# Performance work log

Measured on AMD Instinct MI355X. Metric: run time of the kernel, lower is better.

Reference implementation:

```python
import jax, jax.numpy as jnp
import numpy as np

NEG_BIG = -1e10
EPS = 1e-12  # F.normalize default eps


def l2_normalize(x, axis=-1):
    # matches torch.nn.functional.normalize(x): x / max(||x||_2, eps)
    n = jnp.sqrt(jnp.sum(x * x, axis=axis, keepdims=True))
    return x / jnp.maximum(n, EPS)


def setup_inputs() -> dict:
    key = jax.random.key(0)
    k1, k2, k3 = jax.random.split(key, 3)
    B, S, T, D, R = 16, 512, 512, 512, 8
    return {
        "src_emb": jax.random.normal(k1, (B, S, D), dtype=jnp.float32),
        "tar_emb": jax.random.normal(k2, (B, T, D), dtype=jnp.float32),
        "src_mask": jnp.ones((B, S), dtype=jnp.float32),
        "tar_mask": jnp.ones((B, T), dtype=jnp.float32),
        "mul_score_w": jax.random.normal(k3, (R, D), dtype=jnp.float32),
    }


def reference(src_emb, tar_emb, src_mask, tar_mask, mul_score_w):
    # w: [R, D] row-normalized relation vectors
    w = l2_normalize(mul_score_w, axis=-1)
    # rank-1 diagonal projections per relation
    src_wt = jnp.einsum("bsd,rd->brs", src_emb, w)          # [B,R,S]
    tar_wt = jnp.einsum("btd,rd->brt", tar_emb, w)          # [B,R,T]
    src_map = src_wt[..., None] * w[None, :, None, :]        # [B,R,S,D]
    tar_map = tar_wt[..., None] * w[None, :, None, :]        # [B,R,T,D]
    # attention scores per relation
    score = jnp.einsum("brsd,brtd->brst", src_map, tar_map)  # [B,R,S,T]
    pair_mask = src_mask[:, :, None] * tar_mask[:, None, :]  # [B,S,T]
    score = score + ((1.0 - pair_mask) * NEG_BIG)[:, None, :, :]
    weight = jax.nn.softmax(score, axis=3)                   # softmax over tar
    # sum over rel and tar in one contraction (avoids 5D tensor)
    out = jnp.einsum("brst,brtd->bsd", weight, tar_map)      # [B,S,D]
    return out
```

## Files before the change

kernel.cpp:

```cpp
#include <hip/hip_runtime.h>
#include <hip/hip_bf16.h>
#include <math.h>

#define B 16
#define Sn 512
#define Tn 512
#define Dn 512
#define Rn 8
#define NEG_BIG (-1e10f)

__device__ __forceinline__ float wred_sum(float v) {
#pragma unroll
  for (int off = 32; off; off >>= 1) v += __shfl_xor(v, off, 64);
  return v;
}
__device__ __forceinline__ float wred_max(float v) {
#pragma unroll
  for (int off = 32; off; off >>= 1) v = fmaxf(v, __shfl_xor(v, off, 64));
  return v;
}

__device__ __forceinline__ void stage_norm_w(const float* __restrict__ w,
                                             float4* w4n, float* gs) {
  const float4* wg = (const float4*)w;
  int wid = threadIdx.x >> 6, lane = threadIdx.x & 63;
  int base = wid * 256;
  float4 g0 = wg[base + lane];
  float4 g1 = wg[base + 64 + lane];
  float4 g2 = wg[base + 128 + lane];
  float4 g3 = wg[base + 192 + lane];
  float ss0 = g0.x * g0.x + g0.y * g0.y + g0.z * g0.z + g0.w * g0.w +
              g1.x * g1.x + g1.y * g1.y + g1.z * g1.z + g1.w * g1.w;
  float ss1 = g2.x * g2.x + g2.y * g2.y + g2.z * g2.z + g2.w * g2.w +
              g3.x * g3.x + g3.y * g3.y + g3.z * g3.z + g3.w * g3.w;
  ss0 = wred_sum(ss0);
  ss1 = wred_sum(ss1);
  float inv0 = 1.0f / fmaxf(sqrtf(ss0), 1e-12f);
  float inv1 = 1.0f / fmaxf(sqrtf(ss1), 1e-12f);
  float4 o;
  o.x = g0.x * inv0; o.y = g0.y * inv0; o.z = g0.z * inv0; o.w = g0.w * inv0;
  w4n[base + lane] = o;
  o.x = g1.x * inv0; o.y = g1.y * inv0; o.z = g1.z * inv0; o.w = g1.w * inv0;
  w4n[base + 64 + lane] = o;
  o.x = g2.x * inv1; o.y = g2.y * inv1; o.z = g2.z * inv1; o.w = g2.w * inv1;
  w4n[base + 128 + lane] = o;
  o.x = g3.x * inv1; o.y = g3.y * inv1; o.z = g3.z * inv1; o.w = g3.w * inv1;
  w4n[base + 192 + lane] = o;
  if (lane == 0) {
    gs[2 * wid] = ss0 * inv0 * inv0;
    gs[2 * wid + 1] = ss1 * inv1 * inv1;
  }
}

__global__ __launch_bounds__(256) void proj_kernel(
    const float* __restrict__ src_emb, const float* __restrict__ tar_emb,
    const float* __restrict__ w, float* __restrict__ src_wt,
    float* __restrict__ tar_wt) {
  __shared__ float4 w4n[Rn * 128];
  __shared__ float gs[Rn];
  stage_norm_w(w, w4n, gs);
  __syncthreads();

  bool is_src = blockIdx.x < 2048;
  const float* emb = is_src ? src_emb : tar_emb;
  float* wt = is_src ? src_wt : tar_wt;
  int bb = is_src ? blockIdx.x : blockIdx.x - 2048;

  int wid = threadIdx.x >> 6, lane = threadIdx.x & 63;
  int row = bb * 4 + wid;
  const float4* e4 = (const float4*)(emb + (size_t)row * Dn);
  float4 xa = e4[lane];
  float4 xb = e4[lane + 64];

  float p[8];
#pragma unroll
  for (int r = 0; r < 8; ++r) {
    float4 wa = w4n[r * 128 + lane];
    float4 wb = w4n[r * 128 + 64 + lane];
    p[r] = xa.x * wa.x + xa.y * wa.y + xa.z * wa.z + xa.w * wa.w +
           xb.x * wb.x + xb.y * wb.y + xb.z * wb.z + xb.w * wb.w;
  }
#pragma unroll
  for (int off = 32; off; off >>= 1) {
#pragma unroll
    for (int r = 0; r < 8; ++r) p[r] += __shfl_xor(p[r], off, 64);
  }
  if (lane == 0) {
    int b = row >> 9, n = row & 511;
#pragma unroll
    for (int r = 0; r < 8; ++r) wt[(((size_t)b * Rn + r) << 9) + n] = p[r];
  }
}

__global__ __launch_bounds__(256) void fused_kernel(
    const float* __restrict__ src_wt, const float* __restrict__ tar_wt,
    const float* __restrict__ src_mask, const float* __restrict__ tar_mask,
    const float* __restrict__ w, float* __restrict__ out) {
  __shared__ float4 w4n[Rn * 128];
  __shared__ float gs[Rn];
  __shared__ float sw_s[Rn][8];
  __shared__ float sm_s[8];

  int b = blockIdx.x >> 6;
  int s0 = (blockIdx.x & 63) * 8;

  stage_norm_w(w, w4n, gs);
  if (threadIdx.x < 64) {
    int r = threadIdx.x >> 3, si = threadIdx.x & 7;
    sw_s[r][si] = src_wt[(((size_t)b * Rn + r) << 9) + s0 + si];
    if (r == 0) sm_s[si] = src_mask[((size_t)b << 9) + s0 + si];
  }
  __syncthreads();

  int wid = threadIdx.x >> 6, lane = threadIdx.x & 63;

  const float4* twb = (const float4*)(tar_wt + ((size_t)b << 12));
  float4 tw[8][2];
#pragma unroll
  for (int r = 0; r < 8; ++r) {
    tw[r][0] = twb[r * 128 + lane];
    tw[r][1] = twb[r * 128 + 64 + lane];
  }
  const float4* tmb = (const float4*)(tar_mask + ((size_t)b << 9));
  float4 tm0 = tmb[lane], tm1 = tmb[lane + 64];
  float gr[8];
#pragma unroll
  for (int r = 0; r < 8; ++r) gr[r] = gs[r];

#pragma unroll
  for (int it = 0; it < 2; ++it) {
    int sl = wid * 2 + it;
    int s = s0 + sl;
    float sm = sm_s[sl];
    float mk[8];
    mk[0] = (1.0f - sm * tm0.x) * NEG_BIG;
    mk[1] = (1.0f - sm * tm0.y) * NEG_BIG;
    mk[2] = (1.0f - sm * tm0.z) * NEG_BIG;
    mk[3] = (1.0f - sm * tm0.w) * NEG_BIG;
    mk[4] = (1.0f - sm * tm1.x) * NEG_BIG;
    mk[5] = (1.0f - sm * tm1.y) * NEG_BIG;
    mk[6] = (1.0f - sm * tm1.z) * NEG_BIG;
    mk[7] = (1.0f - sm * tm1.w) * NEG_BIG;

    float cacc[8];
#pragma unroll
    for (int r = 0; r < 8; ++r) {
      float a = gr[r] * sw_s[r][sl];
      float twv[8] = {tw[r][0].x, tw[r][0].y, tw[r][0].z, tw[r][0].w,
                      tw[r][1].x, tw[r][1].y, tw[r][1].z, tw[r][1].w};
      float sc[8];
      float m = -INFINITY;
#pragma unroll
      for (int k = 0; k < 8; ++k) {
        sc[k] = a * twv[k] + mk[k];
        m = fmaxf(m, sc[k]);
      }
      m = wred_max(m);
      float ps = 0.f, wsum = 0.f;
#pragma unroll
      for (int k = 0; k < 8; ++k) {
        float p = __expf(sc[k] - m);
        ps += p;
        wsum += p * twv[k];
      }
      ps = wred_sum(ps);
      wsum = wred_sum(wsum);
      cacc[r] = wsum / ps;
    }

    float4 o0 = {0, 0, 0, 0}, o1 = {0, 0, 0, 0};
#pragma unroll
    for (int r = 0; r < 8; ++r) {
      float4 wa = w4n[r * 128 + lane];
      float4 wb = w4n[r * 128 + 64 + lane];
      o0.x += cacc[r] * wa.x; o0.y += cacc[r] * wa.y;
      o0.z += cacc[r] * wa.z; o0.w += cacc[r] * wa.w;
      o1.x += cacc[r] * wb.x; o1.y += cacc[r] * wb.y;
      o1.z += cacc[r] * wb.z; o1.w += cacc[r] * wb.w;
    }
    float4* dst = (float4*)(out + (((size_t)b << 9) + s) * Dn);
    dst[lane] = o0;
    dst[lane + 64] = o1;
  }
}

extern "C" void kernel_launch(void* const* d_in, const int* in_sizes, int n_in,
                              void* d_out, int out_size, void* d_ws,
                              size_t ws_size, hipStream_t stream) {
  const float* src_emb = (const float*)d_in[0];
  const float* tar_emb = (const float*)d_in[1];
  const float* src_mask = (const float*)d_in[2];
  const float* tar_mask = (const float*)d_in[3];
  const float* w_in = (const float*)d_in[4];
  float* out = (float*)d_out;

  float* ws = (float*)d_ws;
  float* src_wt = ws;
  float* tar_wt = ws + 65536;

  proj_kernel<<<4096, 256, 0, stream>>>(src_emb, tar_emb, w_in, src_wt, tar_wt);
  fused_kernel<<<B * 64, 256, 0, stream>>>(src_wt, tar_wt, src_mask, tar_mask,
                                           w_in, out);
}
```

Baseline: 116.8 us.

## Rewrite projection and softmax kernels with bound-based max and register weights

Both kernels are restructured. The projection kernel handles four rows per wave, keeps the normalized weights in registers instead of LDS, uses a folding shuffle reduction across the 8 relations, and writes a [row, R] layout. The fused kernel stages target projections in LDS, replaces the per-row max reduction with an analytic upper bound |a|*max|tw| so softmax needs one pass with exp2, and gives each lane one (s, r) pair looping over T. This removes many cross-lane max/sum reductions and LDS traffic. The bound-based shift could underflow when |a|*M is large, and each block now recomputes the weight normalization redundantly.

```diff
diff --git a/kernel.cpp b/kernel.cpp
--- a/kernel.cpp
+++ b/kernel.cpp
@@ -8,47 +8,61 @@
 #define Dn 512
 #define Rn 8
 #define NEG_BIG (-1e10f)
-
-__device__ __forceinline__ float wred_sum(float v) {
-#pragma unroll
-  for (int off = 32; off; off >>= 1) v += __shfl_xor(v, off, 64);
+#define L2E 1.4426950408889634f
+
+__device__ __forceinline__ float dot4(float4 a, float4 b) {
+  return a.x * b.x + a.y * b.y + a.z * b.z + a.w * b.w;
+}
+
+__device__ __forceinline__ float fold_reduce8(const float* p, int lane) {
+  bool b0 = lane & 1;
+  float q[4];
+#pragma unroll
+  for (int j = 0; j < 4; ++j) {
+    float s = b0 ? p[2 * j] : p[2 * j + 1];
+    float rv = __shfl_xor(s, 1, 64);
+    q[j] = (b0 ? p[2 * j + 1] : p[2 * j]) + rv;
+  }
+  bool b1 = lane & 2;
+  float u[2];
+#pragma unroll
+  for (int j = 0; j < 2; ++j) {
+    float s = b1 ? q[2 * j] : q[2 * j + 1];
+    float rv = __shfl_xor(s, 2, 64);
+    u[j] = (b1 ? q[2 * j + 1] : q[2 * j]) + rv;
+  }
+  bool b2 = lane & 4;
+  float s = b2 ? u[0] : u[1];
+  float rv = __shfl_xor(s, 4, 64);
+  float v = (b2 ? u[1] : u[0]) + rv;
+  v += __shfl_xor(v, 8, 64);
+  v += __shfl_xor(v, 16, 64);
+  v += __shfl_xor(v, 32, 64);
   return v;
 }
-__device__ __forceinline__ float wred_max(float v) {
-#pragma unroll
-  for (int off = 32; off; off >>= 1) v = fmaxf(v, __shfl_xor(v, off, 64));
-  return v;
-}
-
-__device__ __forceinline__ void stage_norm_w(const float* __restrict__ w,
-                                             float4* w4n, float* gs) {
+
+__device__ __forceinline__ void load_norm_w(const float* __restrict__ w,
+                                            int lane, float4* wa, float4* wb,
+                                            float* g) {
   const float4* wg = (const float4*)w;
-  int wid = threadIdx.x >> 6, lane = threadIdx.x & 63;
-  int base = wid * 256;
-  float4 g0 = wg[base + lane];
-  float4 g1 = wg[base + 64 + lane];
-  float4 g2 = wg[base + 128 + lane];
-  float4 g3 = wg[base + 192 + lane];
-  float ss0 = g0.x * g0.x + g0.y * g0.y + g0.z * g0.z + g0.w * g0.w +
-              g1.x * g1.x + g1.y * g1.y + g1.z * g1.z + g1.w * g1.w;
-  float ss1 = g2.x * g2.x + g2.y * g2.y + g2.z * g2.z + g2.w * g2.w +
-              g3.x * g3.x + g3.y * g3.y + g3.z * g3.z + g3.w * g3.w;
-  ss0 = wred_sum(ss0);
-  ss1 = wred_sum(ss1);
-  float inv0 = 1.0f / fmaxf(sqrtf(ss0), 1e-12f);
-  float inv1 = 1.0f / fmaxf(sqrtf(ss1), 1e-12f);
-  float4 o;
-  o.x = g0.x * inv0; o.y = g0.y * inv0; o.z = g0.z * inv0; o.w = g0.w * inv0;
-  w4n[base + lane] = o;
-  o.x = g1.x * inv0; o.y = g1.y * inv0; o.z = g1.z * inv0; o.w = g1.w * inv0;
-  w4n[base + 64 + lane] = o;
-  o.x = g2.x * inv1; o.y = g2.y * inv1; o.z = g2.z * inv1; o.w = g2.w * inv1;
-  w4n[base + 128 + lane] = o;
-  o.x = g3.x * inv1; o.y = g3.y * inv1; o.z = g3.z * inv1; o.w = g3.w * inv1;
-  w4n[base + 192 + lane] = o;
-  if (lane == 0) {
-    gs[2 * wid] = ss0 * inv0 * inv0;
-    gs[2 * wid + 1] = ss1 * inv1 * inv1;
+  float ss[8];
+#pragma unroll
+  for (int r = 0; r < 8; ++r) {
+    wa[r] = wg[r * 128 + lane];
+    wb[r] = wg[r * 128 + 64 + lane];
+    ss[r] = dot4(wa[r], wa[r]) + dot4(wb[r], wb[r]);
+  }
+#pragma unroll
+  for (int off = 32; off; off >>= 1) {
+#pragma unroll
+    for (int r = 0; r < 8; ++r) ss[r] += __shfl_xor(ss[r], off, 64);
+  }
+#pragma unroll
+  for (int r = 0; r < 8; ++r) {
+    float iv = 1.0f / fmaxf(sqrtf(ss[r]), 1e-12f);
+    wa[r].x *= iv; wa[r].y *= iv; wa[r].z *= iv; wa[r].w *= iv;
+    wb[r].x *= iv; wb[r].y *= iv; wb[r].z *= iv; wb[r].w *= iv;
+    g[r] = ss[r] * iv * iv;
   }
 }
 
@@ -56,39 +70,32 @@
     const float* __restrict__ src_emb, const float* __restrict__ tar_emb,
     const float* __restrict__ w, float* __restrict__ src_wt,
     float* __restrict__ tar_wt) {
-  __shared__ float4 w4n[Rn * 128];
-  __shared__ float gs[Rn];
-  stage_norm_w(w, w4n, gs);
-  __syncthreads();
-
-  bool is_src = blockIdx.x < 2048;
+  int lane = threadIdx.x & 63, wid = threadIdx.x >> 6;
+  float4 wa[8], wb[8];
+  float g[8];
+  load_norm_w(w, lane, wa, wb, g);
+
+  int row0 = blockIdx.x * 16 + wid * 4;
+  bool is_src = row0 < B * Sn;
   const float* emb = is_src ? src_emb : tar_emb;
   float* wt = is_src ? src_wt : tar_wt;
-  int bb = is_src ? blockIdx.x : blockIdx.x - 2048;
-
-  int wid = threadIdx.x >> 6, lane = threadIdx.x & 63;
-  int row = bb * 4 + wid;
-  const float4* e4 = (const float4*)(emb + (size_t)row * Dn);
-  float4 xa = e4[lane];
-  float4 xb = e4[lane + 64];
-
-  float p[8];
-#pragma unroll
-  for (int r = 0; r < 8; ++r) {
-    float4 wa = w4n[r * 128 + lane];
-    float4 wb = w4n[r * 128 + 64 + lane];
-    p[r] = xa.x * wa.x + xa.y * wa.y + xa.z * wa.z + xa.w * wa.w +
-           xb.x * wb.x + xb.y * wb.y + xb.z * wb.z + xb.w * wb.w;
-  }
-#pragma unroll
-  for (int off = 32; off; off >>= 1) {
-#pragma unroll
-    for (int r = 0; r < 8; ++r) p[r] += __shfl_xor(p[r], off, 64);
-  }
-  if (lane == 0) {
-    int b = row >> 9, n = row & 511;
-#pragma unroll
-    for (int r = 0; r < 8; ++r) wt[(((size_t)b * Rn + r) << 9) + n] = p[r];
+  int rb = is_src ? row0 : row0 - B * Sn;
+
+  float v[4];
+#pragma unroll
+  for (int i = 0; i < 4; ++i) {
+    const float4* e4 = (const float4*)(emb + (size_t)(rb + i) * Dn);
+    float4 xa = e4[lane];
+    float4 xb = e4[64 + lane];
+    float p[8];
+#pragma unroll
+    for (int r = 0; r < 8; ++r) p[r] = dot4(xa, wa[r]) + dot4(xb, wb[r]);
+    v[i] = fold_reduce8(p, lane);
+  }
+  if (lane < 32) {
+    int ri = lane >> 3;
+    float val = (ri == 0) ? v[0] : (ri == 1) ? v[1] : (ri == 2) ? v[2] : v[3];
+    wt[(size_t)(rb + ri) * 8 + (lane & 7)] = val;
   }
 }
 
@@ -96,91 +103,91 @@
     const float* __restrict__ src_wt, const float* __restrict__ tar_wt,
     const float* __restrict__ src_mask, const float* __restrict__ tar_mask,
     const float* __restrict__ w, float* __restrict__ out) {
-  __shared__ float4 w4n[Rn * 128];
-  __shared__ float gs[Rn];
-  __shared__ float sw_s[Rn][8];
-  __shared__ float sm_s[8];
-
-  int b = blockIdx.x >> 6;
-  int s0 = (blockIdx.x & 63) * 8;
-
-  stage_norm_w(w, w4n, gs);
-  if (threadIdx.x < 64) {
-    int r = threadIdx.x >> 3, si = threadIdx.x & 7;
-    sw_s[r][si] = src_wt[(((size_t)b * Rn + r) << 9) + s0 + si];
-    if (r == 0) sm_s[si] = src_mask[((size_t)b << 9) + s0 + si];
-  }
+  __shared__ __align__(16) float tw_lds[Tn * 12];
+  __shared__ float tm_lds[Tn];
+  __shared__ __align__(16) float cacc_lds[16 * 8];
+  __shared__ float mred[4];
+
+  int lane = threadIdx.x & 63, wid = threadIdx.x >> 6;
+  int b = blockIdx.x >> 5;
+  int s0 = (blockIdx.x & 31) * 16;
+
+  float4 wa[8], wb[8];
+  float g[8];
+  load_norm_w(w, lane, wa, wb, g);
+
+  const float4* twg = (const float4*)(tar_wt + (size_t)b * Tn * 8);
+  float mloc = 0.0f;
+#pragma unroll
+  for (int k = 0; k < 4; ++k) {
+    int idx = k * 256 + threadIdx.x;
+    float4 vv = twg[idx];
+    int t = idx >> 1, hf = idx & 1;
+    *(float4*)&tw_lds[t * 12 + hf * 4] = vv;
+    mloc = fmaxf(mloc, fmaxf(fmaxf(fabsf(vv.x), fabsf(vv.y)),
+                             fmaxf(fabsf(vv.z), fabsf(vv.w))));
+  }
+  for (int k = threadIdx.x; k < Tn; k += 256)
+    tm_lds[k] = tar_mask[b * Tn + k];
+#pragma unroll
+  for (int off = 32; off; off >>= 1)
+    mloc = fmaxf(mloc, __shfl_xor(mloc, off, 64));
+  if (lane == 0) mred[wid] = mloc;
   __syncthreads();
-
-  int wid = threadIdx.x >> 6, lane = threadIdx.x & 63;
-
-  const float4* twb = (const float4*)(tar_wt + ((size_t)b << 12));
-  float4 tw[8][2];
-#pragma unroll
-  for (int r = 0; r < 8; ++r) {
-    tw[r][0] = twb[r * 128 + lane];
-    tw[r][1] = twb[r * 128 + 64 + lane];
-  }
-  const float4* tmb = (const float4*)(tar_mask + ((size_t)b << 9));
-  float4 tm0 = tmb[lane], tm1 = tmb[lane + 64];
-  float gr[8];
-#pragma unroll
-  for (int r = 0; r < 8; ++r) gr[r] = gs[r];
-
-#pragma unroll
-  for (int it = 0; it < 2; ++it) {
-    int sl = wid * 2 + it;
-    int s = s0 + sl;
-    float sm = sm_s[sl];
-    float mk[8];
-    mk[0] = (1.0f - sm * tm0.x) * NEG_BIG;
-    mk[1] = (1.0f - sm * tm0.y) * NEG_BIG;
-    mk[2] = (1.0f - sm * tm0.z) * NEG_BIG;
-    mk[3] = (1.0f - sm * tm0.w) * NEG_BIG;
-    mk[4] = (1.0f - sm * tm1.x) * NEG_BIG;
-    mk[5] = (1.0f - sm * tm1.y) * NEG_BIG;
-    mk[6] = (1.0f - sm * tm1.z) * NEG_BIG;
-    mk[7] = (1.0f - sm * tm1.w) * NEG_BIG;
-
-    float cacc[8];
-#pragma unroll
-    for (int r = 0; r < 8; ++r) {
-      float a = gr[r] * sw_s[r][sl];
-      float twv[8] = {tw[r][0].x, tw[r][0].y, tw[r][0].z, tw[r][0].w,
-                      tw[r][1].x, tw[r][1].y, tw[r][1].z, tw[r][1].w};
-      float sc[8];
-      float m = -INFINITY;
-#pragma unroll
-      for (int k = 0; k < 8; ++k) {
-        sc[k] = a * twv[k] + mk[k];
-        m = fmaxf(m, sc[k]);
-      }
-      m = wred_max(m);
-      float ps = 0.f, wsum = 0.f;
-#pragma unroll
-      for (int k = 0; k < 8; ++k) {
-        float p = __expf(sc[k] - m);
-        ps += p;
-        wsum += p * twv[k];
-      }
-      ps = wred_sum(ps);
-      wsum = wred_sum(wsum);
-      cacc[r] = wsum / ps;
+  float M = fmaxf(fmaxf(mred[0], mred[1]), fmaxf(mred[2], mred[3]));
+
+  int r = lane & 7, h = (lane >> 3) & 1, sl4 = lane >> 4;
+  int s_local = wid * 4 + sl4;
+  int s = s0 + s_local;
+
+  float g_r = (r & 4) ? ((r & 2) ? ((r & 1) ? g[7] : g[6])
+                                 : ((r & 1) ? g[5] : g[4]))
+                      : ((r & 2) ? ((r & 1) ? g[3] : g[2])
+                                 : ((r & 1) ? g[1] : g[0]));
+  float sw = src_wt[((size_t)(b * Sn + s)) * 8 + r];
+  float sm = src_mask[b * Sn + s];
+  float a = g_r * sw;
+  float A2 = a * L2E;
+  float Bm = sm * (-NEG_BIG) * L2E;
+  float C2 = L2E * (sm * NEG_BIG - fabsf(a) * M);
+
+  float ps = 0.0f, wsum = 0.0f;
+  int t0 = h * 256;
+#pragma unroll 8
+  for (int t = t0; t < t0 + 256; ++t) {
+    float tw = tw_lds[t * 12 + r];
+    float tm = tm_lds[t];
+    float sc = fmaf(A2, tw, fmaf(Bm, tm, C2));
+    float p = __builtin_amdgcn_exp2f(sc);
+    ps += p;
+    wsum = fmaf(p, tw, wsum);
+  }
+  ps += __shfl_xor(ps, 8, 64);
+  wsum += __shfl_xor(wsum, 8, 64);
+  if (h == 0) cacc_lds[s_local * 8 + r] = wsum / ps;
+  __syncthreads();
+
+#pragma unroll
+  for (int i = 0; i < 4; ++i) {
+    int srow = wid * 4 + i;
+    float4 c0 = *(const float4*)&cacc_lds[srow * 8];
+    float4 c1 = *(const float4*)&cacc_lds[srow * 8 + 4];
+    float cc[8] = {c0.x, c0.y, c0.z, c0.w, c1.x, c1.y, c1.z, c1.w};
+    float4 o0 = {0, 0, 0, 0}, o1 = {0, 0, 0, 0};
+#pragma unroll
+    for (int rr = 0; rr < 8; ++rr) {
+      o0.x = fmaf(cc[rr], wa[rr].x, o0.x);
+      o0.y = fmaf(cc[rr], wa[rr].y, o0.y);
+      o0.z = fmaf(cc[rr], wa[rr].z, o0.z);
+      o0.w = fmaf(cc[rr], wa[rr].w, o0.w);
+      o1.x = fmaf(cc[rr], wb[rr].x, o1.x);
+      o1.y = fmaf(cc[rr], wb[rr].y, o1.y);
+      o1.z = fmaf(cc[rr], wb[rr].z, o1.z);
+      o1.w = fmaf(cc[rr], wb[rr].w, o1.w);
     }
-
-    float4 o0 = {0, 0, 0, 0}, o1 = {0, 0, 0, 0};
-#pragma unroll
-    for (int r = 0; r < 8; ++r) {
-      float4 wa = w4n[r * 128 + lane];
-      float4 wb = w4n[r * 128 + 64 + lane];
-      o0.x += cacc[r] * wa.x; o0.y += cacc[r] * wa.y;
-      o0.z += cacc[r] * wa.z; o0.w += cacc[r] * wa.w;
-      o1.x += cacc[r] * wb.x; o1.y += cacc[r] * wb.y;
-      o1.z += cacc[r] * wb.z; o1.w += cacc[r] * wb.w;
-    }
-    float4* dst = (float4*)(out + (((size_t)b << 9) + s) * Dn);
+    float4* dst = (float4*)(out + (size_t)(b * Sn + s0 + srow) * Dn);
     dst[lane] = o0;
-    dst[lane + 64] = o1;
+    dst[64 + lane] = o1;
   }
 }
 
@@ -198,7 +205,8 @@
   float* src_wt = ws;
   float* tar_wt = ws + 65536;
 
-  proj_kernel<<<4096, 256, 0, stream>>>(src_emb, tar_emb, w_in, src_wt, tar_wt);
-  fused_kernel<<<B * 64, 256, 0, stream>>>(src_wt, tar_wt, src_mask, tar_mask,
-                                           w_in, out);
-}
+  proj_kernel<<<(B * (Sn + Tn)) / 16, 256, 0, stream>>>(src_emb, tar_emb, w_in,
+                                                        src_wt, tar_wt);
+  fused_kernel<<<B * (Sn / 16), 256, 0, stream>>>(src_wt, tar_wt, src_mask,
+                                                  tar_mask, w_in, out);
+}
```

Result: faster. 102.3 us (-12.4%).
